# Kernel tuning notes

Hardware: AMD Instinct MI355X
Metric: run time of the kernel (lower is better)

The kernel has to match this reference:

```python
import jax, jax.numpy as jnp
from jax import lax
import numpy as np

N_ITERS = 200        # FISTA iterations (replaces per-row CVXPY solves)
BISECT_ITERS = 50    # bisection steps for capped-simplex projection
POWER_ITERS = 30     # power iterations for Lipschitz estimate


def _project_capped_simplex(v, lower, upper):
    """Project v (shape [N]) onto {x : sum(x)=1, lower<=x<=upper} via bisection on the dual shift tau."""
    lo = jnp.min(v) - upper
    hi = jnp.max(v) - lower

    def body(carry, _):
        lo, hi = carry
        mid = 0.5 * (lo + hi)
        s = jnp.sum(jnp.clip(v - mid, lower, upper))  # decreasing in mid
        lo = jnp.where(s > 1.0, mid, lo)
        hi = jnp.where(s > 1.0, hi, mid)
        return (lo, hi), None

    (lo, hi), _ = lax.scan(body, (lo, hi), None, length=BISECT_ITERS)
    tau = 0.5 * (lo + hi)
    return jnp.clip(v - tau, lower, upper)


def _solve_qp_batched(A, Y, lower, upper):
    """Batched solve of min_x ||x @ A - y||^2 s.t. sum(x)=1, lower<=x<=upper,
    one QP per row y of Y. A: [N,D], Y: [N,D] -> X: [N,N]. FISTA with exact
    capped-simplex projection; faithful to the per-row CVXPY QP in the source."""
    N = A.shape[0]
    Q = A @ A.T            # [N,N] Hessian/2
    C = Y @ A.T            # [N,N] linear term

    # Lipschitz constant of gradient = 2 * lambda_max(Q), via power iteration.
    v = jnp.ones((N,), A.dtype) / N

    def pw(v, _):
        w = Q @ v
        return w / (jnp.linalg.norm(w) + 1e-12), None

    v, _ = lax.scan(pw, v, None, length=POWER_ITERS)
    lmax = v @ (Q @ v)
    step = 1.0 / (2.0 * lmax + 1e-12)

    proj = jax.vmap(lambda r: _project_capped_simplex(r, lower, upper))
    X0 = jnp.full((N, N), 1.0 / N, A.dtype)  # feasible start (uniform simplex point)

    def fista(carry, _):
        X, Z, t = carry
        G = 2.0 * (Z @ Q - C)                 # grad of ||z A - y||^2 wrt z, all rows at once
        Xn = proj(Z - step * G)
        tn = 0.5 * (1.0 + jnp.sqrt(1.0 + 4.0 * t * t))
        Zn = Xn + ((t - 1.0) / tn) * (Xn - X)
        return (Xn, Zn, tn), None

    (X, _, _), _ = lax.scan(fista, (X0, X0, jnp.asarray(1.0, A.dtype)), None, length=N_ITERS)
    return X


def setup_inputs() -> dict:
    key = jax.random.key(0)
    k1, k2 = jax.random.split(key)
    N, D = 2048, 512
    fea1 = jax.random.normal(k1, (N, D), jnp.float32)
    fea2 = jax.random.normal(k2, (N, D), jnp.float32)
    return {"fea1": fea1, "fea2": fea2}


def reference(fea1, fea2):
    lower, upper = 0.0, 1.0
    nfea1 = fea1 / jnp.linalg.norm(fea1, axis=1, keepdims=True)
    nfea2 = fea2 / jnp.linalg.norm(fea2, axis=1, keepdims=True)
    # Solver operates on detached features in the original (numpy/CVXPY).
    XX = _solve_qp_batched(lax.stop_gradient(nfea2), lax.stop_gradient(nfea1), lower, upper)
    XX = lax.stop_gradient(XX)  # mirrors XX.detach() in the source
    distance = -jnp.mean((XX @ nfea2 - nfea1) ** 2)  # -MSELoss
    return distance
```

## Files before the change

kernel.cpp:

```cpp
#include <hip/hip_runtime.h>
#include <cmath>

#define N 2048
#define D 512
#define N_ITERS 200
#define NEWTON_ITERS 12
#define POWER_ITERS 30

typedef unsigned short u16;
typedef __bf16 bf16x8 __attribute__((ext_vector_type(8)));
typedef float f32x4 __attribute__((ext_vector_type(4)));

__device__ __forceinline__ float wave_reduce_sum(float x) {
#pragma unroll
  for (int o = 32; o > 0; o >>= 1) x += __shfl_xor(x, o, 64);
  return x;
}

__device__ __forceinline__ u16 f2b(float f) {
  unsigned int u = __float_as_uint(f);
  u = (u + 0x7FFFu + ((u >> 16) & 1u)) >> 16;
  return (u16)u;
}

__device__ __forceinline__ float b2f(unsigned int lo16) {
  return __uint_as_float((lo16 & 0xffffu) << 16);
}

__device__ __forceinline__ void gload16(const u16* g, u16* l) {
  __builtin_amdgcn_global_load_lds(
      (const __attribute__((address_space(1))) unsigned int*)g,
      (__attribute__((address_space(3))) unsigned int*)l, 16, 0, 0);
}

__device__ __forceinline__ int xcd_swz(int bid) { return (bid & 7) * 32 + (bid >> 3); }

__global__ __launch_bounds__(256) void rownorm_kernel(const float* __restrict__ fea1,
                                                      const float* __restrict__ fea2,
                                                      float* __restrict__ Y,
                                                      u16* __restrict__ Yb,
                                                      float* __restrict__ A) {
  int b = blockIdx.x;
  int row = b & (N - 1);
  const float* src = (b < N) ? fea1 : fea2;
  float* dst = (b < N) ? Y : A;
  const float2* s2 = (const float2*)(src + (size_t)row * D);
  float2* d2 = (float2*)(dst + (size_t)row * D);
  int t = threadIdx.x;
  float2 v = s2[t];
  float ss = v.x * v.x + v.y * v.y;
  ss = wave_reduce_sum(ss);
  __shared__ float sred[4];
  int wid = t >> 6, lane = t & 63;
  if (lane == 0) sred[wid] = ss;
  __syncthreads();
  if (t == 0) sred[0] = sred[0] + sred[1] + sred[2] + sred[3];
  __syncthreads();
  float inv = 1.0f / sqrtf(sred[0]);
  float2 o = make_float2(v.x * inv, v.y * inv);
  d2[t] = o;
  if (b < N) {
    unsigned int pk = (unsigned int)f2b(o.x) | ((unsigned int)f2b(o.y) << 16);
    *(unsigned int*)&Yb[(size_t)row * D + t * 2] = pk;
  }
}

__global__ __launch_bounds__(256) void prep_kernel(const float* __restrict__ A,
                                                   u16* __restrict__ Ab,
                                                   u16* __restrict__ AbT) {
  __shared__ float tile[32][33];
  int c0 = blockIdx.x * 32, r0 = blockIdx.y * 32;
  int tid = threadIdx.x;
  int r = tid >> 3, q = tid & 7;
  float4 v = *(const float4*)&A[(size_t)(r0 + r) * D + c0 + q * 4];
  tile[r][q * 4 + 0] = v.x; tile[r][q * 4 + 1] = v.y;
  tile[r][q * 4 + 2] = v.z; tile[r][q * 4 + 3] = v.w;
  ushort4 b4 = make_ushort4(f2b(v.x), f2b(v.y), f2b(v.z), f2b(v.w));
  *(ushort4*)&Ab[(size_t)(r0 + r) * D + c0 + q * 4] = b4;
  __syncthreads();
  int c = tid >> 3, qq = tid & 7;
  ushort4 t4 = make_ushort4(f2b(tile[qq * 4 + 0][c]), f2b(tile[qq * 4 + 1][c]),
                            f2b(tile[qq * 4 + 2][c]), f2b(tile[qq * 4 + 3][c]));
  *(ushort4*)&AbT[(size_t)(c0 + c) * N + r0 + qq * 4] = t4;
}

__global__ __launch_bounds__(256) void fill_init(u16* __restrict__ Zb, u16* __restrict__ Xb) {
  const unsigned int cw = (unsigned int)f2b(1.0f / (float)N);
  const unsigned int pp = cw | (cw << 16);
  size_t i = (size_t)blockIdx.x * blockDim.x + threadIdx.x;
  uint4 val = make_uint4(pp, pp, pp, pp);
  ((uint4*)Zb)[i] = val;
  ((uint4*)Xb)[i] = val;
}

__global__ __launch_bounds__(256) void ata_kernel(const u16* __restrict__ AbT,
                                                  u16* __restrict__ Mb) {
  __shared__ float Ts[64][17];
  __shared__ float As[64][17];
  const int tid = threadIdx.x;
  const int row0 = blockIdx.y * 64, col0 = blockIdx.x * 64;
  const int tx = tid & 15, ty = tid >> 4;
  const int lr = tid >> 2;
  const int lk = (tid & 3) * 4;
  float acc[4][4] = {};
  for (int k0 = 0; k0 < N; k0 += 16) {
    ushort4 t4 = *(const ushort4*)(AbT + (size_t)(row0 + lr) * N + k0 + lk);
    ushort4 a4 = *(const ushort4*)(AbT + (size_t)(col0 + lr) * N + k0 + lk);
    Ts[lr][lk + 0] = b2f(t4.x); Ts[lr][lk + 1] = b2f(t4.y);
    Ts[lr][lk + 2] = b2f(t4.z); Ts[lr][lk + 3] = b2f(t4.w);
    As[lr][lk + 0] = b2f(a4.x); As[lr][lk + 1] = b2f(a4.y);
    As[lr][lk + 2] = b2f(a4.z); As[lr][lk + 3] = b2f(a4.w);
    __syncthreads();
#pragma unroll
    for (int kk = 0; kk < 16; ++kk) {
      float ar[4], br[4];
#pragma unroll
      for (int i = 0; i < 4; ++i) ar[i] = Ts[ty * 4 + i][kk];
#pragma unroll
      for (int j = 0; j < 4; ++j) br[j] = As[tx * 4 + j][kk];
#pragma unroll
      for (int i = 0; i < 4; ++i)
#pragma unroll
        for (int j = 0; j < 4; ++j) acc[i][j] = fmaf(ar[i], br[j], acc[i][j]);
    }
    __syncthreads();
  }
#pragma unroll
  for (int i = 0; i < 4; ++i) {
    int r = row0 + ty * 4 + i;
#pragma unroll
    for (int j = 0; j < 4; ++j) {
      int c = col0 + tx * 4 + j;
      Mb[(size_t)r * D + c] = f2b(acc[i][j]);
    }
  }
}

__global__ __launch_bounds__(512) void powerM_kernel(const u16* __restrict__ Mb,
                                                     float* __restrict__ sp) {
  __shared__ float v[D];
  __shared__ float r1[8], r2[8];
  const int tid = threadIdx.x;
  v[tid] = 1.0f;
  __syncthreads();
  for (int it = 0; it < POWER_ITERS; ++it) {
    float acc = 0.f;
#pragma unroll 8
    for (int k = 0; k < D; ++k) acc = fmaf(b2f(Mb[(size_t)k * D + tid]), v[k], acc);
    __syncthreads();
    v[tid] = acc * 0.0625f;
    __syncthreads();
  }
  float acc = 0.f;
#pragma unroll 8
  for (int k = 0; k < D; ++k) acc = fmaf(b2f(Mb[(size_t)k * D + tid]), v[k], acc);
  float vi = v[tid];
  float num = wave_reduce_sum(vi * acc);
  float den = wave_reduce_sum(vi * vi);
  int wid = tid >> 6, lane = tid & 63;
  if (lane == 0) { r1[wid] = num; r2[wid] = den; }
  __syncthreads();
  if (tid == 0) {
    float t1 = 0.f, t2 = 0.f;
#pragma unroll
    for (int i = 0; i < 8; ++i) { t1 += r1[i]; t2 += r2[i]; }
    float lam = t1 / t2;
    sp[0] = 1.0f / (2.0f * lam + 1e-12f);
  }
}


template <int FOUT>
__global__ __launch_bounds__(256) void gemm1_mfma(const u16* __restrict__ Am,
                                                  const u16* __restrict__ Bm,
                                                  const u16* __restrict__ Yb,
                                                  const float* __restrict__ Y,
                                                  u16* __restrict__ outb,
                                                  float* __restrict__ outf) {
  __shared__ u16 lds[2 * 16384];
  const int work = xcd_swz(blockIdx.x), tid = threadIdx.x;
  const int lane = tid & 63, wid = tid >> 6;
  const int row0 = (work >> 3) * 64, col0 = (work & 7) * 64;
  const int wr = (wid >> 1) * 32, wc = (wid & 1) * 32;
  const int fr = lane & 15, h = lane >> 4;
  const int grow = lane >> 4, gslot = lane & 15;
  f32x4 acc[2][2] = {};

#define G1S(BUF, T)                                                              \
  {                                                                              \
    const int k0 = (T) * 128;                                                    \
    _Pragma("unroll") for (int q = 0; q < 4; ++q) {                              \
      const int m = wid * 4 + q;                                                 \
      const int r = m * 4 + grow;                                                \
      const int kl = (gslot ^ (r & 15)) * 8;                                     \
      gload16(&Am[(size_t)(row0 + r) * 2048 + k0 + kl], &lds[(BUF)*16384 + m*512]);        \
      gload16(&Bm[(size_t)(col0 + r) * 2048 + k0 + kl], &lds[(BUF)*16384 + 8192 + m*512]); \
    }                                                                            \
  }

  G1S(0, 0);
  __syncthreads();
#pragma unroll 2
  for (int t = 0; t < 16; ++t) {
    const int buf = (t & 1) * 16384;
    if (t < 15) G1S((t & 1) ^ 1, t + 1);
    bf16x8 af[2][4], bg[2][4];
#pragma unroll
    for (int i = 0; i < 2; ++i) {
      const int r = wr + i * 16 + fr;
#pragma unroll
      for (int ks = 0; ks < 4; ++ks)
        af[i][ks] = *(const bf16x8*)&lds[buf + r * 128 + ((((ks << 2) + h) ^ (r & 15)) << 3)];
    }
#pragma unroll
    for (int j = 0; j < 2; ++j) {
      const int c = wc + j * 16 + fr;
#pragma unroll
      for (int ks = 0; ks < 4; ++ks)
        bg[j][ks] = *(const bf16x8*)&lds[buf + 8192 + c * 128 + ((((ks << 2) + h) ^ (c & 15)) << 3)];
    }
#pragma unroll
    for (int ks = 0; ks < 4; ++ks)
#pragma unroll
      for (int i = 0; i < 2; ++i)
#pragma unroll
        for (int j = 0; j < 2; ++j)
          acc[i][j] = __builtin_amdgcn_mfma_f32_16x16x32_bf16(af[i][ks], bg[j][ks], acc[i][j], 0, 0, 0);
    __syncthreads();
  }
#pragma unroll
  for (int i = 0; i < 2; ++i)
#pragma unroll
    for (int j = 0; j < 2; ++j)
#pragma unroll
      for (int g = 0; g < 4; ++g) {
        int r = row0 + wr + i * 16 + h * 4 + g;
        int c = col0 + wc + j * 16 + fr;
        if (FOUT) outf[(size_t)r * D + c] = acc[i][j][g] - Y[(size_t)r * D + c];
        else      outb[(size_t)r * D + c] = f2b(acc[i][j][g] - b2f(Yb[(size_t)r * D + c]));
      }
#undef G1S
}

__global__ __launch_bounds__(256) void gemm2_mfma(const u16* __restrict__ Tb,
                                                  const u16* __restrict__ Ab,
                                                  const u16* __restrict__ Zb,
                                                  const float* __restrict__ sp,
                                                  u16* __restrict__ Vb) {
  __shared__ u16 lds[2 * 16384];
  const int work = xcd_swz(blockIdx.x), tid = threadIdx.x;
  const int lane = tid & 63, wid = tid >> 6;
  const int row0 = (work >> 4) * 128, col0 = (work & 15) * 128;
  const int wr = (wid >> 1) * 64, wc = (wid & 1) * 64;
  const int fr = lane & 15, h = lane >> 4;
  const int grow = lane >> 3, gslot = lane & 7;
  f32x4 acc[4][4] = {};

#define G2S(BUF, T)                                                              \
  {                                                                              \
    const int k0 = (T) * 64;                                                     \
    _Pragma("unroll") for (int q = 0; q < 4; ++q) {                              \
      const int m = wid * 4 + q;                                                 \
      const int r = m * 8 + grow;                                                \
      const int kl = (gslot ^ (r & 7)) * 8;                                      \
      gload16(&Tb[(size_t)(row0 + r) * 512 + k0 + kl], &lds[(BUF)*16384 + m*512]);         \
      gload16(&Ab[(size_t)(col0 + r) * 512 + k0 + kl], &lds[(BUF)*16384 + 8192 + m*512]);  \
    }                                                                            \
  }

  G2S(0, 0);
  __syncthreads();
#pragma unroll 2
  for (int t = 0; t < 8; ++t) {
    const int buf = (t & 1) * 16384;
    if (t < 7) G2S((t & 1) ^ 1, t + 1);
    bf16x8 af[4][2], bg[4][2];
#pragma unroll
    for (int i = 0; i < 4; ++i) {
      const int r = wr + i * 16 + fr;
#pragma unroll
      for (int ks = 0; ks < 2; ++ks)
        af[i][ks] = *(const bf16x8*)&lds[buf + r * 64 + ((((ks << 2) + h) ^ (r & 7)) << 3)];
    }
#pragma unroll
    for (int j = 0; j < 4; ++j) {
      const int c = wc + j * 16 + fr;
#pragma unroll
      for (int ks = 0; ks < 2; ++ks)
        bg[j][ks] = *(const bf16x8*)&lds[buf + 8192 + c * 64 + ((((ks << 2) + h) ^ (c & 7)) << 3)];
    }
#pragma unroll
    for (int ks = 0; ks < 2; ++ks)
#pragma unroll
      for (int i = 0; i < 4; ++i)
#pragma unroll
        for (int j = 0; j < 4; ++j)
          acc[i][j] = __builtin_amdgcn_mfma_f32_16x16x32_bf16(af[i][ks], bg[j][ks], acc[i][j], 0, 0, 0);
    __syncthreads();
  }
  const float s2 = 2.0f * sp[0];
#pragma unroll
  for (int i = 0; i < 4; ++i)
#pragma unroll
    for (int j = 0; j < 4; ++j)
#pragma unroll
      for (int g = 0; g < 4; ++g) {
        int r = row0 + wr + i * 16 + h * 4 + g;
        int c = col0 + wc + j * 16 + fr;
        size_t idx = (size_t)r * N + c;
        Vb[idx] = f2b(b2f(Zb[idx]) - s2 * acc[i][j][g]);
      }
#undef G2S
}

__global__ __launch_bounds__(256) void prox_kernel(const u16* __restrict__ Vb,
                                                   u16* __restrict__ Zb,
                                                   u16* __restrict__ Xb,
                                                   float beta) {
  const int wid = threadIdx.x >> 6, lane = threadIdx.x & 63;
  const int row = blockIdx.x * 4 + wid;
  const size_t rb = (size_t)row * N;
  float v[32], xo[32];
  float mx = -1e30f;
#pragma unroll
  for (int c = 0; c < 4; ++c) {
    const int base = c * 512 + lane * 8;
    uint4 vu = *(const uint4*)&Vb[rb + base];
    uint4 xu = *(const uint4*)&Xb[rb + base];
    const unsigned int vw[4] = {vu.x, vu.y, vu.z, vu.w};
    const unsigned int xw[4] = {xu.x, xu.y, xu.z, xu.w};
#pragma unroll
    for (int w = 0; w < 4; ++w) {
      int e = c * 8 + w * 2;
      float v0 = b2f(vw[w]);
      float v1 = __uint_as_float(vw[w] & 0xffff0000u);
      v[e] = v0; v[e + 1] = v1;
      xo[e] = b2f(xw[w]); xo[e + 1] = __uint_as_float(xw[w] & 0xffff0000u);
      mx = fmaxf(mx, fmaxf(v0, v1));
    }
  }
#pragma unroll
  for (int o = 32; o > 0; o >>= 1) mx = fmaxf(mx, __shfl_xor(mx, o, 64));
  float lo = mx - 1.0f, hi = mx;
  float mid = mx - 0.5f;
#pragma unroll 1
  for (int it = 0; it < NEWTON_ITERS; ++it) {
    float s = 0.f, cnt = 0.f;
#pragma unroll
    for (int e = 0; e < 32; ++e) {
      float d = v[e] - mid;
      float m = __builtin_amdgcn_fmed3f(d, 0.f, 1.f);
      s += m;
      cnt += (m == d) ? 1.f : 0.f;
    }
    s = wave_reduce_sum(s);
    cnt = wave_reduce_sum(cnt);
    bool gt = s > 1.0f;
    lo = gt ? mid : lo;
    hi = gt ? hi : mid;
    float prop = mid + (s - 1.0f) / fmaxf(cnt, 0.5f);
    mid = (prop > lo && prop < hi) ? prop : 0.5f * (lo + hi);
  }
  float tau = mid;
#pragma unroll
  for (int c = 0; c < 4; ++c) {
    const int base = c * 512 + lane * 8;
    unsigned int xp[4], zp[4];
#pragma unroll
    for (int q = 0; q < 8; ++q) {
      int e = c * 8 + q;
      float x = __builtin_amdgcn_fmed3f(v[e] - tau, 0.f, 1.f);
      float zn = x + beta * (x - xo[e]);
      unsigned int xb = (unsigned int)f2b(x);
      unsigned int zb = (unsigned int)f2b(zn);
      if (q & 1) { xp[q >> 1] |= xb << 16; zp[q >> 1] |= zb << 16; }
      else       { xp[q >> 1] = xb;        zp[q >> 1] = zb; }
    }
    *(uint4*)&Xb[rb + base] = make_uint4(xp[0], xp[1], xp[2], xp[3]);
    *(uint4*)&Zb[rb + base] = make_uint4(zp[0], zp[1], zp[2], zp[3]);
  }
}

__global__ void zero_out_kernel(float* __restrict__ out) {
  if (threadIdx.x == 0 && blockIdx.x == 0) out[0] = 0.f;
}

__global__ __launch_bounds__(256) void mse_reduce_kernel(const float* __restrict__ T,
                                                         float* __restrict__ out) {
  size_t i = (size_t)blockIdx.x * blockDim.x + threadIdx.x;
  size_t total = (size_t)N * D;
  size_t stride = (size_t)gridDim.x * blockDim.x;
  float acc = 0.f;
  for (size_t idx = i; idx < total; idx += stride) {
    float t = T[idx];
    acc = fmaf(t, t, acc);
  }
  acc = wave_reduce_sum(acc);
  __shared__ float sred[4];
  int wid = threadIdx.x >> 6, lane = threadIdx.x & 63;
  if (lane == 0) sred[wid] = acc;
  __syncthreads();
  if (threadIdx.x == 0) {
    float tot = sred[0] + sred[1] + sred[2] + sred[3];
    atomicAdd(out, -tot / (float)((size_t)N * D));
  }
}

extern "C" void kernel_launch(void* const* d_in, const int* in_sizes, int n_in,
                              void* d_out, int out_size, void* d_ws, size_t ws_size,
                              hipStream_t stream) {
  const float* fea1 = (const float*)d_in[0];
  const float* fea2 = (const float*)d_in[1];
  float* out = (float*)d_out;
  float* ws = (float*)d_ws;

  float* A   = ws;
  float* Y   = A + (size_t)N * D;
  float* T32 = Y + (size_t)N * D;
  float* sp  = T32 + (size_t)N * D;
  u16* Zb    = (u16*)(sp + 8);
  u16* Vb    = Zb + (size_t)N * N;
  u16* Xb    = Vb + (size_t)N * N;
  u16* Tb    = Xb + (size_t)N * N;
  u16* Ab    = Tb + (size_t)N * D;
  u16* AbT   = Ab + (size_t)N * D;
  u16* Yb    = AbT + (size_t)D * N;
  u16* Mb    = Yb + (size_t)N * D;

  rownorm_kernel<<<2 * N, 256, 0, stream>>>(fea1, fea2, Y, Yb, A);
  prep_kernel<<<dim3(D / 32, N / 32), 256, 0, stream>>>(A, Ab, AbT);
  fill_init<<<(N * N / 8) / 256, 256, 0, stream>>>(Zb, Xb);

  ata_kernel<<<dim3(D / 64, D / 64), 256, 0, stream>>>(AbT, Mb);
  powerM_kernel<<<1, 512, 0, stream>>>(Mb, sp);

  float t = 1.0f;
  for (int it = 0; it < N_ITERS; ++it) {
    float tn = 0.5f * (1.0f + sqrtf(1.0f + 4.0f * t * t));
    float beta = (t - 1.0f) / tn;
    t = tn;
    gemm1_mfma<0><<<256, 256, 0, stream>>>(Zb, AbT, Yb, Y, Tb, T32);
    gemm2_mfma<<<256, 256, 0, stream>>>(Tb, Ab, Zb, sp, Vb);
    prox_kernel<<<N / 4, 256, 0, stream>>>(Vb, Zb, Xb, beta);
  }

  gemm1_mfma<1><<<256, 256, 0, stream>>>(Xb, AbT, Yb, Y, Tb, T32);
  zero_out_kernel<<<1, 64, 0, stream>>>(out);
  mse_reduce_kernel<<<512, 256, 0, stream>>>(T32, out);
}
```

Measured before the change: 9.281 ms.

## Fold the two per-iteration gradient GEMMs into one GEMM with precomputed W

Precomputes W = I - 2*step*A*A^T (N×N, bf16) and a scaled bf16 copy of Y once, before the loop. Each FISTA iteration then computes the gradient step as a single GEMM over a concatenated K = N + D, namely Z·W + (2*step*Y)·A^T. This replaces the previous pair of GEMMs that went through an intermediate T. It cuts one kernel launch and the intermediate round trip per iteration, but each iteration now does about 2.5x the matrix FLOPs. Storing the near-identity W in bf16 also loses precision.

```diff
diff --git a/kernel.cpp b/kernel.cpp
--- a/kernel.cpp
+++ b/kernel.cpp
@@ -38,7 +38,6 @@
 __global__ __launch_bounds__(256) void rownorm_kernel(const float* __restrict__ fea1,
                                                       const float* __restrict__ fea2,
                                                       float* __restrict__ Y,
-                                                      u16* __restrict__ Yb,
                                                       float* __restrict__ A) {
   int b = blockIdx.x;
   int row = b & (N - 1);
@@ -57,12 +56,7 @@
   if (t == 0) sred[0] = sred[0] + sred[1] + sred[2] + sred[3];
   __syncthreads();
   float inv = 1.0f / sqrtf(sred[0]);
-  float2 o = make_float2(v.x * inv, v.y * inv);
-  d2[t] = o;
-  if (b < N) {
-    unsigned int pk = (unsigned int)f2b(o.x) | ((unsigned int)f2b(o.y) << 16);
-    *(unsigned int*)&Yb[(size_t)row * D + t * 2] = pk;
-  }
+  d2[t] = make_float2(v.x * inv, v.y * inv);
 }
 
 __global__ __launch_bounds__(256) void prep_kernel(const float* __restrict__ A,
@@ -169,13 +163,231 @@
   }
 }
 
-
-template <int FOUT>
-__global__ __launch_bounds__(256) void gemm1_mfma(const u16* __restrict__ Am,
+__global__ __launch_bounds__(256) void wgemm_mfma(const u16* __restrict__ Ab,
+                                                  const float* __restrict__ sp,
+                                                  u16* __restrict__ Wb) {
+  __shared__ u16 lds[2 * 16384];
+  const int work = xcd_swz(blockIdx.x), tid = threadIdx.x;
+  const int lane = tid & 63, wid = tid >> 6;
+  const int row0 = (work >> 4) * 128, col0 = (work & 15) * 128;
+  const int wr = (wid >> 1) * 64, wc = (wid & 1) * 64;
+  const int fr = lane & 15, h = lane >> 4;
+  const int grow = lane >> 3, gslot = lane & 7;
+  f32x4 acc[4][4] = {};
+
+#define WS(BUF, T)                                                               \
+  {                                                                              \
+    const int k0 = (T) * 64;                                                     \
+    _Pragma("unroll") for (int q = 0; q < 4; ++q) {                              \
+      const int m = wid * 4 + q;                                                 \
+      const int r = m * 8 + grow;                                                \
+      const int kl = (gslot ^ (r & 7)) * 8;                                      \
+      gload16(&Ab[(size_t)(row0 + r) * 512 + k0 + kl], &lds[(BUF)*16384 + m*512]);         \
+      gload16(&Ab[(size_t)(col0 + r) * 512 + k0 + kl], &lds[(BUF)*16384 + 8192 + m*512]);  \
+    }                                                                            \
+  }
+
+  WS(0, 0);
+  __syncthreads();
+#pragma unroll 2
+  for (int t = 0; t < 8; ++t) {
+    const int buf = (t & 1) * 16384;
+    if (t < 7) WS((t & 1) ^ 1, t + 1);
+    bf16x8 af[4][2], bg[4][2];
+#pragma unroll
+    for (int i = 0; i < 4; ++i) {
+      const int r = wr + i * 16 + fr;
+#pragma unroll
+      for (int ks = 0; ks < 2; ++ks)
+        af[i][ks] = *(const bf16x8*)&lds[buf + r * 64 + ((((ks << 2) + h) ^ (r & 7)) << 3)];
+    }
+#pragma unroll
+    for (int j = 0; j < 4; ++j) {
+      const int c = wc + j * 16 + fr;
+#pragma unroll
+      for (int ks = 0; ks < 2; ++ks)
+        bg[j][ks] = *(const bf16x8*)&lds[buf + 8192 + c * 64 + ((((ks << 2) + h) ^ (c & 7)) << 3)];
+    }
+#pragma unroll
+    for (int ks = 0; ks < 2; ++ks)
+#pragma unroll
+      for (int i = 0; i < 4; ++i)
+#pragma unroll
+        for (int j = 0; j < 4; ++j)
+          acc[i][j] = __builtin_amdgcn_mfma_f32_16x16x32_bf16(af[i][ks], bg[j][ks], acc[i][j], 0, 0, 0);
+    __syncthreads();
+  }
+  const float s2 = 2.0f * sp[0];
+#pragma unroll
+  for (int i = 0; i < 4; ++i)
+#pragma unroll
+    for (int j = 0; j < 4; ++j)
+#pragma unroll
+      for (int g = 0; g < 4; ++g) {
+        int r = row0 + wr + i * 16 + h * 4 + g;
+        int c = col0 + wc + j * 16 + fr;
+        float diag = (r == c) ? 1.0f : 0.0f;
+        Wb[(size_t)r * N + c] = f2b(diag - s2 * acc[i][j][g]);
+      }
+#undef WS
+}
+
+__global__ __launch_bounds__(256) void yscale_kernel(const float* __restrict__ Y,
+                                                     const float* __restrict__ sp,
+                                                     u16* __restrict__ Ysb) {
+  const float s2 = 2.0f * sp[0];
+  size_t i = ((size_t)blockIdx.x * blockDim.x + threadIdx.x) * 4;
+  float4 y = *(const float4*)&Y[i];
+  *(ushort4*)&Ysb[i] = make_ushort4(f2b(s2 * y.x), f2b(s2 * y.y),
+                                    f2b(s2 * y.z), f2b(s2 * y.w));
+}
+
+__global__ __launch_bounds__(256) void vgemm_mfma(const u16* __restrict__ Zb,
+                                                  const u16* __restrict__ Ysb,
+                                                  const u16* __restrict__ Wb,
+                                                  const u16* __restrict__ Ab,
+                                                  u16* __restrict__ Vb) {
+  __shared__ u16 lds[2 * 16384];
+  const int work = xcd_swz(blockIdx.x), tid = threadIdx.x;
+  const int lane = tid & 63, wid = tid >> 6;
+  const int row0 = (work >> 4) * 128, col0 = (work & 15) * 128;
+  const int wr = (wid >> 1) * 64, wc = (wid & 1) * 64;
+  const int fr = lane & 15, h = lane >> 4;
+  const int grow = lane >> 3, gslot = lane & 7;
+  f32x4 acc[4][4] = {};
+
+#define VS(BUF, T)                                                               \
+  {                                                                              \
+    const int k0 = (T) * 64;                                                     \
+    _Pragma("unroll") for (int q = 0; q < 4; ++q) {                              \
+      const int m = wid * 4 + q;                                                 \
+      const int r = m * 8 + grow;                                                \
+      const int kl = (gslot ^ (r & 7)) * 8;                                      \
+      const u16* asrc = (k0 < 2048)                                              \
+          ? &Zb[(size_t)(row0 + r) * 2048 + k0 + kl]                             \
+          : &Ysb[(size_t)(row0 + r) * 512 + (k0 - 2048) + kl];                   \
+      const u16* bsrc = (k0 < 2048)                                              \
+          ? &Wb[(size_t)(col0 + r) * 2048 + k0 + kl]                             \
+          : &Ab[(size_t)(col0 + r) * 512 + (k0 - 2048) + kl];                    \
+      gload16(asrc, &lds[(BUF)*16384 + m*512]);                                  \
+      gload16(bsrc, &lds[(BUF)*16384 + 8192 + m*512]);                           \
+    }                                                                            \
+  }
+
+  VS(0, 0);
+  __syncthreads();
+#pragma unroll 2
+  for (int t = 0; t < 40; ++t) {
+    const int buf = (t & 1) * 16384;
+    if (t < 39) VS((t & 1) ^ 1, t + 1);
+    bf16x8 af[4][2], bg[4][2];
+#pragma unroll
+    for (int i = 0; i < 4; ++i) {
+      const int r = wr + i * 16 + fr;
+#pragma unroll
+      for (int ks = 0; ks < 2; ++ks)
+        af[i][ks] = *(const bf16x8*)&lds[buf + r * 64 + ((((ks << 2) + h) ^ (r & 7)) << 3)];
+    }
+#pragma unroll
+    for (int j = 0; j < 4; ++j) {
+      const int c = wc + j * 16 + fr;
+#pragma unroll
+      for (int ks = 0; ks < 2; ++ks)
+        bg[j][ks] = *(const bf16x8*)&lds[buf + 8192 + c * 64 + ((((ks << 2) + h) ^ (c & 7)) << 3)];
+    }
+#pragma unroll
+    for (int ks = 0; ks < 2; ++ks)
+#pragma unroll
+      for (int i = 0; i < 4; ++i)
+#pragma unroll
+        for (int j = 0; j < 4; ++j)
+          acc[i][j] = __builtin_amdgcn_mfma_f32_16x16x32_bf16(af[i][ks], bg[j][ks], acc[i][j], 0, 0, 0);
+    __syncthreads();
+  }
+#pragma unroll
+  for (int i = 0; i < 4; ++i)
+#pragma unroll
+    for (int j = 0; j < 4; ++j)
+#pragma unroll
+      for (int g = 0; g < 4; ++g) {
+        int r = row0 + wr + i * 16 + h * 4 + g;
+        int c = col0 + wc + j * 16 + fr;
+        Vb[(size_t)r * N + c] = f2b(acc[i][j][g]);
+      }
+#undef VS
+}
+
+__global__ __launch_bounds__(256) void prox_kernel(const u16* __restrict__ Vb,
+                                                   u16* __restrict__ Zb,
+                                                   u16* __restrict__ Xb,
+                                                   float beta) {
+  const int wid = threadIdx.x >> 6, lane = threadIdx.x & 63;
+  const int row = blockIdx.x * 4 + wid;
+  const size_t rb = (size_t)row * N;
+  float v[32], xo[32];
+  float mx = -1e30f;
+#pragma unroll
+  for (int c = 0; c < 4; ++c) {
+    const int base = c * 512 + lane * 8;
+    uint4 vu = *(const uint4*)&Vb[rb + base];
+    uint4 xu = *(const uint4*)&Xb[rb + base];
+    const unsigned int vw[4] = {vu.x, vu.y, vu.z, vu.w};
+    const unsigned int xw[4] = {xu.x, xu.y, xu.z, xu.w};
+#pragma unroll
+    for (int w = 0; w < 4; ++w) {
+      int e = c * 8 + w * 2;
+      float v0 = b2f(vw[w]);
+      float v1 = __uint_as_float(vw[w] & 0xffff0000u);
+      v[e] = v0; v[e + 1] = v1;
+      xo[e] = b2f(xw[w]); xo[e + 1] = __uint_as_float(xw[w] & 0xffff0000u);
+      mx = fmaxf(mx, fmaxf(v0, v1));
+    }
+  }
+#pragma unroll
+  for (int o = 32; o > 0; o >>= 1) mx = fmaxf(mx, __shfl_xor(mx, o, 64));
+  float lo = mx - 1.0f, hi = mx;
+  float mid = mx - 0.5f;
+#pragma unroll 1
+  for (int it = 0; it < NEWTON_ITERS; ++it) {
+    float s = 0.f, cnt = 0.f;
+#pragma unroll
+    for (int e = 0; e < 32; ++e) {
+      float d = v[e] - mid;
+      float m = __builtin_amdgcn_fmed3f(d, 0.f, 1.f);
+      s += m;
+      cnt += (m == d) ? 1.f : 0.f;
+    }
+    s = wave_reduce_sum(s);
+    cnt = wave_reduce_sum(cnt);
+    bool gt = s > 1.0f;
+    lo = gt ? mid : lo;
+    hi = gt ? hi : mid;
+    float prop = mid + (s - 1.0f) / fmaxf(cnt, 0.5f);
+    mid = (prop > lo && prop < hi) ? prop : 0.5f * (lo + hi);
+  }
+  float tau = mid;
+#pragma unroll
+  for (int c = 0; c < 4; ++c) {
+    const int base = c * 512 + lane * 8;
+    unsigned int xp[4], zp[4];
+#pragma unroll
+    for (int q = 0; q < 8; ++q) {
+      int e = c * 8 + q;
+      float x = __builtin_amdgcn_fmed3f(v[e] - tau, 0.f, 1.f);
+      float zn = x + beta * (x - xo[e]);
+      unsigned int xb = (unsigned int)f2b(x);
+      unsigned int zb = (unsigned int)f2b(zn);
+      if (q & 1) { xp[q >> 1] |= xb << 16; zp[q >> 1] |= zb << 16; }
+      else       { xp[q >> 1] = xb;        zp[q >> 1] = zb; }
+    }
+    *(uint4*)&Xb[rb + base] = make_uint4(xp[0], xp[1], xp[2], xp[3]);
+    *(uint4*)&Zb[rb + base] = make_uint4(zp[0], zp[1], zp[2], zp[3]);
+  }
+}
+
+__global__ __launch_bounds__(256) void tgemm_mfma(const u16* __restrict__ Am,
                                                   const u16* __restrict__ Bm,
-                                                  const u16* __restrict__ Yb,
                                                   const float* __restrict__ Y,
-                                                  u16* __restrict__ outb,
                                                   float* __restrict__ outf) {
   __shared__ u16 lds[2 * 16384];
   const int work = xcd_swz(blockIdx.x), tid = threadIdx.x;
@@ -186,7 +398,7 @@
   const int grow = lane >> 4, gslot = lane & 15;
   f32x4 acc[2][2] = {};
 
-#define G1S(BUF, T)                                                              \
+#define TS(BUF, T)                                                               \
   {                                                                              \
     const int k0 = (T) * 128;                                                    \
     _Pragma("unroll") for (int q = 0; q < 4; ++q) {                              \
@@ -198,12 +410,12 @@
     }                                                                            \
   }
 
-  G1S(0, 0);
+  TS(0, 0);
   __syncthreads();
 #pragma unroll 2
   for (int t = 0; t < 16; ++t) {
     const int buf = (t & 1) * 16384;
-    if (t < 15) G1S((t & 1) ^ 1, t + 1);
+    if (t < 15) TS((t & 1) ^ 1, t + 1);
     bf16x8 af[2][4], bg[2][4];
 #pragma unroll
     for (int i = 0; i < 2; ++i) {
@@ -236,149 +448,9 @@
       for (int g = 0; g < 4; ++g) {
         int r = row0 + wr + i * 16 + h * 4 + g;
         int c = col0 + wc + j * 16 + fr;
-        if (FOUT) outf[(size_t)r * D + c] = acc[i][j][g] - Y[(size_t)r * D + c];
-        else      outb[(size_t)r * D + c] = f2b(acc[i][j][g] - b2f(Yb[(size_t)r * D + c]));
+        outf[(size_t)r * D + c] = acc[i][j][g] - Y[(size_t)r * D + c];
       }
-#undef G1S
-}
-
-__global__ __launch_bounds__(256) void gemm2_mfma(const u16* __restrict__ Tb,
-                                                  const u16* __restrict__ Ab,
-                                                  const u16* __restrict__ Zb,
-                                                  const float* __restrict__ sp,
-                                                  u16* __restrict__ Vb) {
-  __shared__ u16 lds[2 * 16384];
-  const int work = xcd_swz(blockIdx.x), tid = threadIdx.x;
-  const int lane = tid & 63, wid = tid >> 6;
-  const int row0 = (work >> 4) * 128, col0 = (work & 15) * 128;
-  const int wr = (wid >> 1) * 64, wc = (wid & 1) * 64;
-  const int fr = lane & 15, h = lane >> 4;
-  const int grow = lane >> 3, gslot = lane & 7;
-  f32x4 acc[4][4] = {};
-
-#define G2S(BUF, T)                                                              \
-  {                                                                              \
-    const int k0 = (T) * 64;                                                     \
-    _Pragma("unroll") for (int q = 0; q < 4; ++q) {                              \
-      const int m = wid * 4 + q;                                                 \
-      const int r = m * 8 + grow;                                                \
-      const int kl = (gslot ^ (r & 7)) * 8;                                      \
-      gload16(&Tb[(size_t)(row0 + r) * 512 + k0 + kl], &lds[(BUF)*16384 + m*512]);         \
-      gload16(&Ab[(size_t)(col0 + r) * 512 + k0 + kl], &lds[(BUF)*16384 + 8192 + m*512]);  \
-    }                                                                            \
-  }
-
-  G2S(0, 0);
-  __syncthreads();
-#pragma unroll 2
-  for (int t = 0; t < 8; ++t) {
-    const int buf = (t & 1) * 16384;
-    if (t < 7) G2S((t & 1) ^ 1, t + 1);
-    bf16x8 af[4][2], bg[4][2];
-#pragma unroll
-    for (int i = 0; i < 4; ++i) {
-      const int r = wr + i * 16 + fr;
-#pragma unroll
-      for (int ks = 0; ks < 2; ++ks)
-        af[i][ks] = *(const bf16x8*)&lds[buf + r * 64 + ((((ks << 2) + h) ^ (r & 7)) << 3)];
-    }
-#pragma unroll
-    for (int j = 0; j < 4; ++j) {
-      const int c = wc + j * 16 + fr;
-#pragma unroll
-      for (int ks = 0; ks < 2; ++ks)
-        bg[j][ks] = *(const bf16x8*)&lds[buf + 8192 + c * 64 + ((((ks << 2) + h) ^ (c & 7)) << 3)];
-    }
-#pragma unroll
-    for (int ks = 0; ks < 2; ++ks)
-#pragma unroll
-      for (int i = 0; i < 4; ++i)
-#pragma unroll
-        for (int j = 0; j < 4; ++j)
-          acc[i][j] = __builtin_amdgcn_mfma_f32_16x16x32_bf16(af[i][ks], bg[j][ks], acc[i][j], 0, 0, 0);
-    __syncthreads();
-  }
-  const float s2 = 2.0f * sp[0];
-#pragma unroll
-  for (int i = 0; i < 4; ++i)
-#pragma unroll
-    for (int j = 0; j < 4; ++j)
-#pragma unroll
-      for (int g = 0; g < 4; ++g) {
-        int r = row0 + wr + i * 16 + h * 4 + g;
-        int c = col0 + wc + j * 16 + fr;
-        size_t idx = (size_t)r * N + c;
-        Vb[idx] = f2b(b2f(Zb[idx]) - s2 * acc[i][j][g]);
-      }
-#undef G2S
-}
-
-__global__ __launch_bounds__(256) void prox_kernel(const u16* __restrict__ Vb,
-                                                   u16* __restrict__ Zb,
-                                                   u16* __restrict__ Xb,
-                                                   float beta) {
-  const int wid = threadIdx.x >> 6, lane = threadIdx.x & 63;
-  const int row = blockIdx.x * 4 + wid;
-  const size_t rb = (size_t)row * N;
-  float v[32], xo[32];
-  float mx = -1e30f;
-#pragma unroll
-  for (int c = 0; c < 4; ++c) {
-    const int base = c * 512 + lane * 8;
-    uint4 vu = *(const uint4*)&Vb[rb + base];
-    uint4 xu = *(const uint4*)&Xb[rb + base];
-    const unsigned int vw[4] = {vu.x, vu.y, vu.z, vu.w};
-    const unsigned int xw[4] = {xu.x, xu.y, xu.z, xu.w};
-#pragma unroll
-    for (int w = 0; w < 4; ++w) {
-      int e = c * 8 + w * 2;
-      float v0 = b2f(vw[w]);
-      float v1 = __uint_as_float(vw[w] & 0xffff0000u);
-      v[e] = v0; v[e + 1] = v1;
-      xo[e] = b2f(xw[w]); xo[e + 1] = __uint_as_float(xw[w] & 0xffff0000u);
-      mx = fmaxf(mx, fmaxf(v0, v1));
-    }
-  }
-#pragma unroll
-  for (int o = 32; o > 0; o >>= 1) mx = fmaxf(mx, __shfl_xor(mx, o, 64));
-  float lo = mx - 1.0f, hi = mx;
-  float mid = mx - 0.5f;
-#pragma unroll 1
-  for (int it = 0; it < NEWTON_ITERS; ++it) {
-    float s = 0.f, cnt = 0.f;
-#pragma unroll
-    for (int e = 0; e < 32; ++e) {
-      float d = v[e] - mid;
-      float m = __builtin_amdgcn_fmed3f(d, 0.f, 1.f);
-      s += m;
-      cnt += (m == d) ? 1.f : 0.f;
-    }
-    s = wave_reduce_sum(s);
-    cnt = wave_reduce_sum(cnt);
-    bool gt = s > 1.0f;
-    lo = gt ? mid : lo;
-    hi = gt ? hi : mid;
-    float prop = mid + (s - 1.0f) / fmaxf(cnt, 0.5f);
-    mid = (prop > lo && prop < hi) ? prop : 0.5f * (lo + hi);
-  }
-  float tau = mid;
-#pragma unroll
-  for (int c = 0; c < 4; ++c) {
-    const int base = c * 512 + lane * 8;
-    unsigned int xp[4], zp[4];
-#pragma unroll
-    for (int q = 0; q < 8; ++q) {
-      int e = c * 8 + q;
-      float x = __builtin_amdgcn_fmed3f(v[e] - tau, 0.f, 1.f);
-      float zn = x + beta * (x - xo[e]);
-      unsigned int xb = (unsigned int)f2b(x);
-      unsigned int zb = (unsigned int)f2b(zn);
-      if (q & 1) { xp[q >> 1] |= xb << 16; zp[q >> 1] |= zb << 16; }
-      else       { xp[q >> 1] = xb;        zp[q >> 1] = zb; }
-    }
-    *(uint4*)&Xb[rb + base] = make_uint4(xp[0], xp[1], xp[2], xp[3]);
-    *(uint4*)&Zb[rb + base] = make_uint4(zp[0], zp[1], zp[2], zp[3]);
-  }
+#undef TS
 }
 
 __global__ void zero_out_kernel(float* __restrict__ out) {
@@ -421,30 +493,32 @@
   u16* Zb    = (u16*)(sp + 8);
   u16* Vb    = Zb + (size_t)N * N;
   u16* Xb    = Vb + (size_t)N * N;
-  u16* Tb    = Xb + (size_t)N * N;
-  u16* Ab    = Tb + (size_t)N * D;
+  u16* Wb    = Xb + (size_t)N * N;
+  u16* Ab    = Wb + (size_t)N * N;
   u16* AbT   = Ab + (size_t)N * D;
-  u16* Yb    = AbT + (size_t)D * N;
-  u16* Mb    = Yb + (size_t)N * D;
-
-  rownorm_kernel<<<2 * N, 256, 0, stream>>>(fea1, fea2, Y, Yb, A);
+  u16* Ysb   = AbT + (size_t)D * N;
+  u16* Mb    = Ysb + (size_t)N * D;
+
+  rownorm_kernel<<<2 * N, 256, 0, stream>>>(fea1, fea2, Y, A);
   prep_kernel<<<dim3(D / 32, N / 32), 256, 0, stream>>>(A, Ab, AbT);
   fill_init<<<(N * N / 8) / 256, 256, 0, stream>>>(Zb, Xb);
 
   ata_kernel<<<dim3(D / 64, D / 64), 256, 0, stream>>>(AbT, Mb);
   powerM_kernel<<<1, 512, 0, stream>>>(Mb, sp);
+
+  wgemm_mfma<<<256, 256, 0, stream>>>(Ab, sp, Wb);
+  yscale_kernel<<<(N * D / 4) / 256, 256, 0, stream>>>(Y, sp, Ysb);
 
   float t = 1.0f;
   for (int it = 0; it < N_ITERS; ++it) {
     float tn = 0.5f * (1.0f + sqrtf(1.0f + 4.0f * t * t));
     float beta = (t - 1.0f) / tn;
     t = tn;
-    gemm1_mfma<0><<<256, 256, 0, stream>>>(Zb, AbT, Yb, Y, Tb, T32);
-    gemm2_mfma<<<256, 256, 0, stream>>>(Tb, Ab, Zb, sp, Vb);
+    vgemm_mfma<<<256, 256, 0, stream>>>(Zb, Ysb, Wb, Ab, Vb);
     prox_kernel<<<N / 4, 256, 0, stream>>>(Vb, Zb, Xb, beta);
   }
 
-  gemm1_mfma<1><<<256, 256, 0, stream>>>(Xb, AbT, Yb, Y, Tb, T32);
+  tgemm_mfma<<<256, 256, 0, stream>>>(Xb, AbT, Y, T32);
   zero_out_kernel<<<1, 64, 0, stream>>>(out);
   mse_reduce_kernel<<<512, 256, 0, stream>>>(T32, out);
 }
```

Result: slower. 11.20 ms (+20.7%).
